# Kernel tuning notes

Hardware: AMD Instinct MI355X
Metric: run time of the kernel (lower is better)

Reference implementation:

```python
import jax, jax.numpy as jnp
import numpy as np

N_NODES = 50000
EMBED = 64
N_EDGES = 1250000
N_USERS = 25000
BATCH, K = 1024, 100


def setup_inputs() -> dict:
    key = jax.random.key(0)
    ks = jax.random.split(key, 8)
    stdv = 1.0 / np.sqrt(EMBED)
    emb = jax.random.uniform(ks[0], (N_NODES, EMBED), jnp.float32, -stdv, stdv)
    # nn.Linear default init: U(-1/sqrt(fan_in), 1/sqrt(fan_in))
    lim = 1.0 / np.sqrt(EMBED)
    W0 = jax.random.uniform(ks[1], (EMBED, EMBED), jnp.float32, -lim, lim)
    b0 = jax.random.uniform(ks[2], (EMBED,), jnp.float32, -lim, lim)
    W1 = jax.random.uniform(ks[3], (EMBED, EMBED), jnp.float32, -lim, lim)
    b1 = jax.random.uniform(ks[4], (EMBED,), jnp.float32, -lim, lim)
    src = jax.random.randint(ks[5], (N_EDGES,), 0, N_NODES, jnp.int32)
    dst = jax.random.randint(ks[6], (N_EDGES,), 0, N_NODES, jnp.int32)
    user_index = jax.random.randint(ks[7], (BATCH, K), 0, N_USERS, jnp.int32)
    item_index = jax.random.randint(jax.random.fold_in(key, 99), (BATCH, K), 0, N_NODES, jnp.int32)
    return {"embeddings": emb, "W0": W0, "b0": b0, "W1": W1, "b1": b1,
            "src": src, "dst": dst, "user_index": user_index, "item_index": item_index}


def _mean_aggregate(h, src, dst):
    # copy_src gather + mailbox mean: mean of src features over incoming edges per dst
    msg_sum = jax.ops.segment_sum(h[src], dst, num_segments=N_NODES)  # [N, D]
    deg = jax.ops.segment_sum(jnp.ones((src.shape[0],), h.dtype), dst, num_segments=N_NODES)
    return msg_sum / jnp.maximum(deg, 1.0)[:, None]


def reference(embeddings, W0, b0, W1, b1, src, dst, user_index, item_index):
    h = embeddings
    for W, b in ((W0, b0), (W1, b1)):
        agg = _mean_aggregate(h, src, dst)          # [N, D] mean mailbox
        h = jnp.tanh(agg @ W.T + b)                  # NodeUpdate: Linear + Tanh
    user = h[user_index]                             # [B, K, D]
    item = h[item_index]                             # [B, K, D]
    score = jnp.sum(user * item, axis=2)             # [B, K]
    return score
```

## Files before the change

### kernel.cpp

```cpp
#include <hip/hip_runtime.h>

#define N_NODES 50000
#define N_EDGES 1250000
#define EMBED 64
#define N_PAIRS (1024 * 100)
#define BSHIFT 7
#define BSIZE 128
#define NBUCK 391
#define CB 153
#define LDS_CAP 4096
#define GEMV_BLKS ((N_NODES + 63) / 64)

__device__ inline float bf2f(unsigned short u) {
    return __uint_as_float(((unsigned)u) << 16);
}
__device__ inline unsigned short f2bf(float x) {
    unsigned u = __float_as_uint(x);
    u += 0x7FFF + ((u >> 16) & 1);
    return (unsigned short)(u >> 16);
}

__global__ __launch_bounds__(1024) void hist_kernel(const int* __restrict__ dst,
                                                    int* __restrict__ counts,
                                                    int* __restrict__ btot) {
    __shared__ int hl[NBUCK];
    int t = threadIdx.x, b = blockIdx.x;
    for (int i = t; i < NBUCK; i += 1024) hl[i] = 0;
    __syncthreads();
    #pragma unroll
    for (int rep = 0; rep < 2; ++rep) {
        int i4 = b * 2048 + rep * 1024 + t;
        if (i4 < N_EDGES / 4) {
            int4 d = ((const int4*)dst)[i4];
            atomicAdd(&hl[d.x >> BSHIFT], 1);
            atomicAdd(&hl[d.y >> BSHIFT], 1);
            atomicAdd(&hl[d.z >> BSHIFT], 1);
            atomicAdd(&hl[d.w >> BSHIFT], 1);
        }
    }
    __syncthreads();
    for (int i = t; i < NBUCK; i += 1024) {
        int v = hl[i];
        counts[i * CB + b] = v;
        if (v) atomicAdd(&btot[i], v);
    }
}

__global__ __launch_bounds__(512) void bscan_kernel(const int* __restrict__ btot,
                                                    int* __restrict__ base) {
    __shared__ int ws[8];
    int t = threadIdx.x, lane = t & 63, wid = t >> 6;
    int v = (t < NBUCK) ? btot[t] : 0;
    int incl = v;
    #pragma unroll
    for (int off = 1; off < 64; off <<= 1) {
        int o = __shfl_up(incl, off);
        if (lane >= off) incl += o;
    }
    if (lane == 63) ws[wid] = incl;
    __syncthreads();
    if (t < 8) {
        int x = ws[t];
        #pragma unroll
        for (int off = 1; off < 8; off <<= 1) {
            int o = __shfl_up(x, off);
            if (t >= off) x += o;
        }
        ws[t] = x;
    }
    __syncthreads();
    int ex = ((wid > 0) ? ws[wid - 1] : 0) + incl - v;
    if (t < NBUCK) base[t] = ex;
    if (t == 0) base[NBUCK] = N_EDGES;
}

__global__ __launch_bounds__(64) void offs_kernel(const int* __restrict__ counts,
                                                  const int* __restrict__ base,
                                                  int* __restrict__ offs) {
    int k = blockIdx.x, lane = threadIdx.x;
    const int* rowp = counts + (size_t)k * CB;
    int* orow = offs + (size_t)k * CB;
    int carry = base[k];
    #pragma unroll
    for (int tile = 0; tile < 3; ++tile) {
        int b = tile * 64 + lane;
        int v = (b < CB) ? rowp[b] : 0;
        int incl = v;
        #pragma unroll
        for (int off = 1; off < 64; off <<= 1) {
            int o = __shfl_up(incl, off);
            if (lane >= off) incl += o;
        }
        if (b < CB) orow[b] = carry + incl - v;
        carry += __shfl(incl, 63);
    }
}

__global__ __launch_bounds__(1024) void scatter_kernel(const int* __restrict__ src,
                                                       const int* __restrict__ dst,
                                                       const int* __restrict__ offs,
                                                       unsigned int* __restrict__ pairs) {
    __shared__ int cur[NBUCK];
    int t = threadIdx.x, b = blockIdx.x;
    for (int i = t; i < NBUCK; i += 1024) cur[i] = offs[i * CB + b];
    __syncthreads();
    #pragma unroll
    for (int rep = 0; rep < 2; ++rep) {
        int i4 = b * 2048 + rep * 1024 + t;
        if (i4 < N_EDGES / 4) {
            int4 s4 = ((const int4*)src)[i4];
            int4 d4 = ((const int4*)dst)[i4];
            int p;
            p = atomicAdd(&cur[d4.x >> BSHIFT], 1);
            pairs[p] = ((unsigned)(d4.x & (BSIZE - 1)) << 16) | (unsigned)s4.x;
            p = atomicAdd(&cur[d4.y >> BSHIFT], 1);
            pairs[p] = ((unsigned)(d4.y & (BSIZE - 1)) << 16) | (unsigned)s4.y;
            p = atomicAdd(&cur[d4.z >> BSHIFT], 1);
            pairs[p] = ((unsigned)(d4.z & (BSIZE - 1)) << 16) | (unsigned)s4.z;
            p = atomicAdd(&cur[d4.w >> BSHIFT], 1);
            pairs[p] = ((unsigned)(d4.w & (BSIZE - 1)) << 16) | (unsigned)s4.w;
        }
    }
}

#define SMEM_BYTES 33808
__global__ __launch_bounds__(256) void sortgemv_kernel(const unsigned int* __restrict__ pairs,
                                                       const int* __restrict__ base,
                                                       int* __restrict__ row,
                                                       int* __restrict__ col,
                                                       const float* __restrict__ emb,
                                                       const float* __restrict__ W,
                                                       unsigned short* __restrict__ g) {
    __shared__ __align__(16) char smem[SMEM_BYTES];
    int t = threadIdx.x;
    if (blockIdx.x < NBUCK) {
        unsigned* ebuf = (unsigned*)smem;
        int* staged    = (int*)(smem + 16384);
        int* hist      = (int*)(smem + 32768);
        int* cur       = (int*)(smem + 33280);
        int* wtot      = (int*)(smem + 33792);
        int k = blockIdx.x;
        int lane = t & 63, wid = t >> 6;
        int nstart = k * BSIZE;
        int nodes = min(BSIZE, N_NODES - nstart);
        int estart = base[k], eend = base[k + 1];
        int cnt = eend - estart;
        if (t < BSIZE) hist[t] = 0;
        __syncthreads();
        if (cnt <= LDS_CAP) {
            for (int i = t; i < cnt; i += 256) {
                unsigned w = pairs[estart + i];
                ebuf[i] = w;
                atomicAdd(&hist[w >> 16], 1);
            }
            __syncthreads();
            if (t < BSIZE) {
                int v = hist[t];
                int incl = v;
                #pragma unroll
                for (int off = 1; off < 64; off <<= 1) {
                    int o = __shfl_up(incl, off);
                    if (lane >= off) incl += o;
                }
                if (t == 63) *wtot = incl;
                __syncthreads();
                int ex = incl - v + ((wid == 1) ? *wtot : 0);
                cur[t] = ex;
                if (t < nodes) row[nstart + t] = estart + ex;
            } else {
                __syncthreads();
            }
            if (k == NBUCK - 1 && t == 0) row[N_NODES] = N_EDGES;
            __syncthreads();
            for (int i = t; i < cnt; i += 256) {
                unsigned w = ebuf[i];
                int pos = atomicAdd(&cur[w >> 16], 1);
                staged[pos] = (int)(w & 0xFFFFu);
            }
            __syncthreads();
            for (int i = t; i < cnt; i += 256) col[estart + i] = staged[i];
        } else {
            for (int i = t; i < cnt; i += 256)
                atomicAdd(&hist[pairs[estart + i] >> 16], 1);
            __syncthreads();
            if (t < BSIZE) {
                int v = hist[t];
                int incl = v;
                #pragma unroll
                for (int off = 1; off < 64; off <<= 1) {
                    int o = __shfl_up(incl, off);
                    if (lane >= off) incl += o;
                }
                if (t == 63) *wtot = incl;
                __syncthreads();
                int ex = incl - v + ((wid == 1) ? *wtot : 0);
                cur[t] = ex;
                if (t < nodes) row[nstart + t] = estart + ex;
            } else {
                __syncthreads();
            }
            if (k == NBUCK - 1 && t == 0) row[N_NODES] = N_EDGES;
            __syncthreads();
            for (int i = t; i < cnt; i += 256) {
                unsigned w = pairs[estart + i];
                int pos = atomicAdd(&cur[w >> 16], 1);
                col[estart + pos] = (int)(w & 0xFFFFu);
            }
        }
    } else {
        float (*hL)[64] = (float (*)[64])smem;
        float (*Wl)[65] = (float (*)[65])(smem + 16384);
        int nstart = (blockIdx.x - NBUCK) * 64;
        int lane = t & 63, wid = t >> 6;
        for (int i = t; i < 4096; i += 256) Wl[i & 63][i >> 6] = W[i];
        int nrem = min(64, N_NODES - nstart);
        for (int i = t; i < nrem * 16; i += 256)
            ((float4*)hL)[i] = ((const float4*)(emb + (size_t)nstart * EMBED))[i];
        __syncthreads();
        for (int n = wid; n < nrem; n += 4) {
            float x = 0.f;
            #pragma unroll
            for (int d = 0; d < 64; ++d)
                x += hL[n][d] * Wl[d][lane];
            g[(size_t)(nstart + n) * EMBED + lane] = f2bf(x);
        }
    }
}

__global__ __launch_bounds__(256) void gemv_bf16_kernel(const unsigned short* __restrict__ h,
                                                        const float* __restrict__ W,
                                                        unsigned short* __restrict__ g) {
    __shared__ float hL[64][64];
    __shared__ float Wl[64][65];
    int t = threadIdx.x;
    int nstart = blockIdx.x * 64;
    int lane = t & 63, wid = t >> 6;
    for (int i = t; i < 4096; i += 256) Wl[i & 63][i >> 6] = W[i];
    int nrem = min(64, N_NODES - nstart);
    for (int i = t; i < nrem * 16; i += 256) {
        ushort4 v = ((const ushort4*)(h + (size_t)nstart * EMBED))[i];
        int r = i >> 4, c = (i & 15) * 4;
        hL[r][c + 0] = bf2f(v.x);
        hL[r][c + 1] = bf2f(v.y);
        hL[r][c + 2] = bf2f(v.z);
        hL[r][c + 3] = bf2f(v.w);
    }
    __syncthreads();
    for (int n = wid; n < nrem; n += 4) {
        float x = 0.f;
        #pragma unroll
        for (int d = 0; d < 64; ++d)
            x += hL[n][d] * Wl[d][lane];
        g[(size_t)(nstart + n) * EMBED + lane] = f2bf(x);
    }
}

__global__ __launch_bounds__(256) void agg_kernel(const unsigned short* __restrict__ g,
                                                  const float* __restrict__ bias,
                                                  const int* __restrict__ row,
                                                  const int* __restrict__ col,
                                                  unsigned short* __restrict__ hout) {
    int t = threadIdx.x;
    int wid = t >> 6, lane = t & 63;
    int node = blockIdx.x * 4 + wid;
    int gg = lane >> 4, d16 = lane & 15;
    int start = row[node], end = row[node + 1];
    float4 bb = ((const float4*)bias)[d16];
    float4 acc = {0.f, 0.f, 0.f, 0.f};
    for (int e = start; e < end; e += 32) {
        #pragma unroll
        for (int k = 0; k < 8; ++k) {
            int ee = e + 4 * k + gg;
            if (ee < end) {
                int s = col[ee];
                ushort4 v = ((const ushort4*)(g + (size_t)s * EMBED))[d16];
                acc.x += bf2f(v.x);
                acc.y += bf2f(v.y);
                acc.z += bf2f(v.z);
                acc.w += bf2f(v.w);
            }
        }
    }
    #pragma unroll
    for (int off = 16; off < 64; off <<= 1) {
        acc.x += __shfl_xor(acc.x, off);
        acc.y += __shfl_xor(acc.y, off);
        acc.z += __shfl_xor(acc.z, off);
        acc.w += __shfl_xor(acc.w, off);
    }
    int dg = end - start;
    float inv = (dg > 0) ? 1.0f / (float)dg : 0.f;
    if (gg == 0) {
        ushort4 o;
        o.x = f2bf(tanhf(acc.x * inv + bb.x));
        o.y = f2bf(tanhf(acc.y * inv + bb.y));
        o.z = f2bf(tanhf(acc.z * inv + bb.z));
        o.w = f2bf(tanhf(acc.w * inv + bb.w));
        ((ushort4*)(hout + (size_t)node * EMBED))[d16] = o;
    }
}

__global__ __launch_bounds__(256) void score_kernel(const unsigned short* __restrict__ h,
                                                    const int* __restrict__ ui,
                                                    const int* __restrict__ ii,
                                                    float* __restrict__ out) {
    int t = threadIdx.x;
    int idx = blockIdx.x * 16 + (t >> 4);
    int d16 = t & 15;
    int u = ui[idx];
    int v = ii[idx];
    ushort4 a4 = ((const ushort4*)(h + (size_t)u * EMBED))[d16];
    ushort4 b4 = ((const ushort4*)(h + (size_t)v * EMBED))[d16];
    float p = bf2f(a4.x) * bf2f(b4.x) + bf2f(a4.y) * bf2f(b4.y) +
              bf2f(a4.z) * bf2f(b4.z) + bf2f(a4.w) * bf2f(b4.w);
    #pragma unroll
    for (int off = 8; off > 0; off >>= 1)
        p += __shfl_xor(p, off);
    if (d16 == 0) out[idx] = p;
}

extern "C" void kernel_launch(void* const* d_in, const int* in_sizes, int n_in,
                              void* d_out, int out_size, void* d_ws, size_t ws_size,
                              hipStream_t stream) {
    const float* emb = (const float*)d_in[0];
    const float* W0  = (const float*)d_in[1];
    const float* b0  = (const float*)d_in[2];
    const float* W1  = (const float*)d_in[3];
    const float* b1  = (const float*)d_in[4];
    const int* src   = (const int*)d_in[5];
    const int* dst   = (const int*)d_in[6];
    const int* ui    = (const int*)d_in[7];
    const int* ii    = (const int*)d_in[8];
    float* out = (float*)d_out;

    char* p = (char*)d_ws;
    auto alloc = [&](size_t bytes) {
        char* r = p;
        p += (bytes + 255) & ~(size_t)255;
        return r;
    };
    int* counts          = (int*)alloc(sizeof(int) * NBUCK * CB);
    int* offs            = (int*)alloc(sizeof(int) * NBUCK * CB);
    int* btot            = (int*)alloc(sizeof(int) * NBUCK);
    int* base            = (int*)alloc(sizeof(int) * (NBUCK + 1));
    int* row             = (int*)alloc(sizeof(int) * (N_NODES + 1));
    unsigned* pairs      = (unsigned*)alloc(sizeof(unsigned) * N_EDGES);
    int* col             = (int*)alloc(sizeof(int) * N_EDGES);
    unsigned short* gbuf = (unsigned short*)alloc(sizeof(unsigned short) * N_NODES * EMBED);
    unsigned short* hbuf = (unsigned short*)alloc(sizeof(unsigned short) * N_NODES * EMBED);

    hipMemsetAsync(btot, 0, sizeof(int) * NBUCK, stream);
    hist_kernel<<<CB, 1024, 0, stream>>>(dst, counts, btot);
    bscan_kernel<<<1, 512, 0, stream>>>(btot, base);
    offs_kernel<<<NBUCK, 64, 0, stream>>>(counts, base, offs);
    scatter_kernel<<<CB, 1024, 0, stream>>>(src, dst, offs, pairs);
    sortgemv_kernel<<<NBUCK + GEMV_BLKS, 256, 0, stream>>>(pairs, base, row, col,
                                                           emb, W0, gbuf);
    agg_kernel<<<N_NODES / 4, 256, 0, stream>>>(gbuf, b0, row, col, hbuf);
    gemv_bf16_kernel<<<GEMV_BLKS, 256, 0, stream>>>(hbuf, W1, gbuf);
    agg_kernel<<<N_NODES / 4, 256, 0, stream>>>(gbuf, b1, row, col, hbuf);
    score_kernel<<<N_PAIRS / 16, 256, 0, stream>>>(hbuf, ui, ii, out);
}
```

Baseline: 245.9 us.

## Switch intermediates to fp32 and pad CSR rows to multiples of four

Drops the bf16 storage of the transformed features and hidden states and keeps everything in fp32. The CSR layout now gives each bucket a fixed region and pads every node's edge list to a multiple of four, filling the padding with a dummy node whose feature row is zero. This removes the per-edge bounds checks in the aggregation loop, which now processes eight edges per step unguarded. The cost is twice the gather bytes from fp32 features, a larger col buffer, and a padding fill pass in the sort kernel.

```diff
diff --git a/kernel.cpp b/kernel.cpp
--- a/kernel.cpp
+++ b/kernel.cpp
@@ -9,16 +9,9 @@
 #define NBUCK 391
 #define CB 153
 #define LDS_CAP 4096
+#define FAST_MAX 3584
+#define CAP 4096
 #define GEMV_BLKS ((N_NODES + 63) / 64)
-
-__device__ inline float bf2f(unsigned short u) {
-    return __uint_as_float(((unsigned)u) << 16);
-}
-__device__ inline unsigned short f2bf(float x) {
-    unsigned u = __float_as_uint(x);
-    u += 0x7FFF + ((u >> 16) & 1);
-    return (unsigned short)(u >> 16);
-}
 
 __global__ __launch_bounds__(1024) void hist_kernel(const int* __restrict__ dst,
                                                     int* __restrict__ counts,
@@ -123,14 +116,15 @@
     }
 }
 
-#define SMEM_BYTES 33808
+#define SMEM_BYTES 34832
 __global__ __launch_bounds__(256) void sortgemv_kernel(const unsigned int* __restrict__ pairs,
                                                        const int* __restrict__ base,
-                                                       int* __restrict__ row,
+                                                       int* __restrict__ rowp,
+                                                       int* __restrict__ degv,
                                                        int* __restrict__ col,
                                                        const float* __restrict__ emb,
                                                        const float* __restrict__ W,
-                                                       unsigned short* __restrict__ g) {
+                                                       float* __restrict__ g) {
     __shared__ __align__(16) char smem[SMEM_BYTES];
     int t = threadIdx.x;
     if (blockIdx.x < NBUCK) {
@@ -139,15 +133,17 @@
         int* hist      = (int*)(smem + 32768);
         int* cur       = (int*)(smem + 33280);
         int* wtot      = (int*)(smem + 33792);
+        int* ptotS     = (int*)(smem + 33796);
         int k = blockIdx.x;
         int lane = t & 63, wid = t >> 6;
         int nstart = k * BSIZE;
         int nodes = min(BSIZE, N_NODES - nstart);
         int estart = base[k], eend = base[k + 1];
         int cnt = eend - estart;
+        int cbase = k << 12;
         if (t < BSIZE) hist[t] = 0;
         __syncthreads();
-        if (cnt <= LDS_CAP) {
+        if (cnt <= FAST_MAX) {
             for (int i = t; i < cnt; i += 256) {
                 unsigned w = pairs[estart + i];
                 ebuf[i] = w;
@@ -155,8 +151,9 @@
             }
             __syncthreads();
             if (t < BSIZE) {
-                int v = hist[t];
-                int incl = v;
+                int dgv = hist[t];
+                int pd = (dgv + 3) & ~3;
+                int incl = pd;
                 #pragma unroll
                 for (int off = 1; off < 64; off <<= 1) {
                     int o = __shfl_up(incl, off);
@@ -164,13 +161,19 @@
                 }
                 if (t == 63) *wtot = incl;
                 __syncthreads();
-                int ex = incl - v + ((wid == 1) ? *wtot : 0);
+                int ex = incl - pd + ((wid == 1) ? *wtot : 0);
                 cur[t] = ex;
-                if (t < nodes) row[nstart + t] = estart + ex;
+                if (t == BSIZE - 1) *ptotS = ex + pd;
+                if (t < nodes) {
+                    rowp[nstart + t] = cbase + ex;
+                    degv[nstart + t] = dgv;
+                }
             } else {
                 __syncthreads();
             }
-            if (k == NBUCK - 1 && t == 0) row[N_NODES] = N_EDGES;
+            __syncthreads();
+            int ptot = *ptotS;
+            for (int i = t; i < ptot; i += 256) staged[i] = N_NODES;
             __syncthreads();
             for (int i = t; i < cnt; i += 256) {
                 unsigned w = ebuf[i];
@@ -178,14 +181,15 @@
                 staged[pos] = (int)(w & 0xFFFFu);
             }
             __syncthreads();
-            for (int i = t; i < cnt; i += 256) col[estart + i] = staged[i];
+            for (int i = t; i < ptot; i += 256) col[cbase + i] = staged[i];
         } else {
             for (int i = t; i < cnt; i += 256)
                 atomicAdd(&hist[pairs[estart + i] >> 16], 1);
             __syncthreads();
             if (t < BSIZE) {
-                int v = hist[t];
-                int incl = v;
+                int dgv = hist[t];
+                int pd = (dgv + 3) & ~3;
+                int incl = pd;
                 #pragma unroll
                 for (int off = 1; off < 64; off <<= 1) {
                     int o = __shfl_up(incl, off);
@@ -193,43 +197,51 @@
                 }
                 if (t == 63) *wtot = incl;
                 __syncthreads();
-                int ex = incl - v + ((wid == 1) ? *wtot : 0);
+                int ex = incl - pd + ((wid == 1) ? *wtot : 0);
                 cur[t] = ex;
-                if (t < nodes) row[nstart + t] = estart + ex;
+                if (t == BSIZE - 1) *ptotS = ex + pd;
+                if (t < nodes) {
+                    rowp[nstart + t] = cbase + ex;
+                    degv[nstart + t] = dgv;
+                }
             } else {
                 __syncthreads();
             }
-            if (k == NBUCK - 1 && t == 0) row[N_NODES] = N_EDGES;
+            __syncthreads();
+            int ptot = *ptotS;
+            for (int i = t; i < ptot; i += 256) col[cbase + i] = N_NODES;
             __syncthreads();
             for (int i = t; i < cnt; i += 256) {
                 unsigned w = pairs[estart + i];
                 int pos = atomicAdd(&cur[w >> 16], 1);
-                col[estart + pos] = (int)(w & 0xFFFFu);
+                col[cbase + pos] = (int)(w & 0xFFFFu);
             }
         }
     } else {
         float (*hL)[64] = (float (*)[64])smem;
         float (*Wl)[65] = (float (*)[65])(smem + 16384);
-        int nstart = (blockIdx.x - NBUCK) * 64;
+        int gb = blockIdx.x - NBUCK;
+        int nstart = gb * 64;
         int lane = t & 63, wid = t >> 6;
         for (int i = t; i < 4096; i += 256) Wl[i & 63][i >> 6] = W[i];
         int nrem = min(64, N_NODES - nstart);
         for (int i = t; i < nrem * 16; i += 256)
             ((float4*)hL)[i] = ((const float4*)(emb + (size_t)nstart * EMBED))[i];
+        if (gb == GEMV_BLKS - 1 && t < 64) g[(size_t)N_NODES * EMBED + t] = 0.f;
         __syncthreads();
         for (int n = wid; n < nrem; n += 4) {
             float x = 0.f;
             #pragma unroll
             for (int d = 0; d < 64; ++d)
                 x += hL[n][d] * Wl[d][lane];
-            g[(size_t)(nstart + n) * EMBED + lane] = f2bf(x);
-        }
-    }
-}
-
-__global__ __launch_bounds__(256) void gemv_bf16_kernel(const unsigned short* __restrict__ h,
-                                                        const float* __restrict__ W,
-                                                        unsigned short* __restrict__ g) {
+            g[(size_t)(nstart + n) * EMBED + lane] = x;
+        }
+    }
+}
+
+__global__ __launch_bounds__(256) void gemv_kernel(const float* __restrict__ h,
+                                                   const float* __restrict__ W,
+                                                   float* __restrict__ g) {
     __shared__ float hL[64][64];
     __shared__ float Wl[64][65];
     int t = threadIdx.x;
@@ -237,49 +249,49 @@
     int lane = t & 63, wid = t >> 6;
     for (int i = t; i < 4096; i += 256) Wl[i & 63][i >> 6] = W[i];
     int nrem = min(64, N_NODES - nstart);
-    for (int i = t; i < nrem * 16; i += 256) {
-        ushort4 v = ((const ushort4*)(h + (size_t)nstart * EMBED))[i];
-        int r = i >> 4, c = (i & 15) * 4;
-        hL[r][c + 0] = bf2f(v.x);
-        hL[r][c + 1] = bf2f(v.y);
-        hL[r][c + 2] = bf2f(v.z);
-        hL[r][c + 3] = bf2f(v.w);
-    }
+    for (int i = t; i < nrem * 16; i += 256)
+        ((float4*)hL)[i] = ((const float4*)(h + (size_t)nstart * EMBED))[i];
     __syncthreads();
     for (int n = wid; n < nrem; n += 4) {
         float x = 0.f;
         #pragma unroll
         for (int d = 0; d < 64; ++d)
             x += hL[n][d] * Wl[d][lane];
-        g[(size_t)(nstart + n) * EMBED + lane] = f2bf(x);
-    }
-}
-
-__global__ __launch_bounds__(256) void agg_kernel(const unsigned short* __restrict__ g,
+        g[(size_t)(nstart + n) * EMBED + lane] = x;
+    }
+}
+
+__global__ __launch_bounds__(256) void agg_kernel(const float* __restrict__ g,
                                                   const float* __restrict__ bias,
-                                                  const int* __restrict__ row,
+                                                  const int* __restrict__ rowp,
+                                                  const int* __restrict__ degv,
                                                   const int* __restrict__ col,
-                                                  unsigned short* __restrict__ hout) {
+                                                  float* __restrict__ hout) {
     int t = threadIdx.x;
     int wid = t >> 6, lane = t & 63;
     int node = blockIdx.x * 4 + wid;
     int gg = lane >> 4, d16 = lane & 15;
-    int start = row[node], end = row[node + 1];
+    int start = rowp[node];
+    int dg = degv[node];
+    int pcnt = (dg + 3) & ~3;
+    int endp = start + pcnt;
     float4 bb = ((const float4*)bias)[d16];
     float4 acc = {0.f, 0.f, 0.f, 0.f};
-    for (int e = start; e < end; e += 32) {
-        #pragma unroll
-        for (int k = 0; k < 8; ++k) {
-            int ee = e + 4 * k + gg;
-            if (ee < end) {
-                int s = col[ee];
-                ushort4 v = ((const ushort4*)(g + (size_t)s * EMBED))[d16];
-                acc.x += bf2f(v.x);
-                acc.y += bf2f(v.y);
-                acc.z += bf2f(v.z);
-                acc.w += bf2f(v.w);
-            }
-        }
+    int e = start;
+    for (; e + 8 <= endp; e += 8) {
+        int s0 = col[e + gg];
+        int s1 = col[e + 4 + gg];
+        float4 v0 = ((const float4*)(g + (size_t)s0 * EMBED))[d16];
+        float4 v1 = ((const float4*)(g + (size_t)s1 * EMBED))[d16];
+        acc.x += v0.x + v1.x;
+        acc.y += v0.y + v1.y;
+        acc.z += v0.z + v1.z;
+        acc.w += v0.w + v1.w;
+    }
+    if (e < endp) {
+        int s0 = col[e + gg];
+        float4 v0 = ((const float4*)(g + (size_t)s0 * EMBED))[d16];
+        acc.x += v0.x; acc.y += v0.y; acc.z += v0.z; acc.w += v0.w;
     }
     #pragma unroll
     for (int off = 16; off < 64; off <<= 1) {
@@ -288,19 +300,18 @@
         acc.z += __shfl_xor(acc.z, off);
         acc.w += __shfl_xor(acc.w, off);
     }
-    int dg = end - start;
     float inv = (dg > 0) ? 1.0f / (float)dg : 0.f;
     if (gg == 0) {
-        ushort4 o;
-        o.x = f2bf(tanhf(acc.x * inv + bb.x));
-        o.y = f2bf(tanhf(acc.y * inv + bb.y));
-        o.z = f2bf(tanhf(acc.z * inv + bb.z));
-        o.w = f2bf(tanhf(acc.w * inv + bb.w));
-        ((ushort4*)(hout + (size_t)node * EMBED))[d16] = o;
-    }
-}
-
-__global__ __launch_bounds__(256) void score_kernel(const unsigned short* __restrict__ h,
+        float4 o;
+        o.x = tanhf(acc.x * inv + bb.x);
+        o.y = tanhf(acc.y * inv + bb.y);
+        o.z = tanhf(acc.z * inv + bb.z);
+        o.w = tanhf(acc.w * inv + bb.w);
+        ((float4*)(hout + (size_t)node * EMBED))[d16] = o;
+    }
+}
+
+__global__ __launch_bounds__(256) void score_kernel(const float* __restrict__ h,
                                                     const int* __restrict__ ui,
                                                     const int* __restrict__ ii,
                                                     float* __restrict__ out) {
@@ -309,10 +320,9 @@
     int d16 = t & 15;
     int u = ui[idx];
     int v = ii[idx];
-    ushort4 a4 = ((const ushort4*)(h + (size_t)u * EMBED))[d16];
-    ushort4 b4 = ((const ushort4*)(h + (size_t)v * EMBED))[d16];
-    float p = bf2f(a4.x) * bf2f(b4.x) + bf2f(a4.y) * bf2f(b4.y) +
-              bf2f(a4.z) * bf2f(b4.z) + bf2f(a4.w) * bf2f(b4.w);
+    float4 a = ((const float4*)(h + (size_t)u * EMBED))[d16];
+    float4 b = ((const float4*)(h + (size_t)v * EMBED))[d16];
+    float p = a.x * b.x + a.y * b.y + a.z * b.z + a.w * b.w;
     #pragma unroll
     for (int off = 8; off > 0; off >>= 1)
         p += __shfl_xor(p, off);
@@ -339,25 +349,26 @@
         p += (bytes + 255) & ~(size_t)255;
         return r;
     };
-    int* counts          = (int*)alloc(sizeof(int) * NBUCK * CB);
-    int* offs            = (int*)alloc(sizeof(int) * NBUCK * CB);
-    int* btot            = (int*)alloc(sizeof(int) * NBUCK);
-    int* base            = (int*)alloc(sizeof(int) * (NBUCK + 1));
-    int* row             = (int*)alloc(sizeof(int) * (N_NODES + 1));
-    unsigned* pairs      = (unsigned*)alloc(sizeof(unsigned) * N_EDGES);
-    int* col             = (int*)alloc(sizeof(int) * N_EDGES);
-    unsigned short* gbuf = (unsigned short*)alloc(sizeof(unsigned short) * N_NODES * EMBED);
-    unsigned short* hbuf = (unsigned short*)alloc(sizeof(unsigned short) * N_NODES * EMBED);
+    int* counts     = (int*)alloc(sizeof(int) * NBUCK * CB);
+    int* offs       = (int*)alloc(sizeof(int) * NBUCK * CB);
+    int* btot       = (int*)alloc(sizeof(int) * NBUCK);
+    int* base       = (int*)alloc(sizeof(int) * (NBUCK + 1));
+    int* rowp       = (int*)alloc(sizeof(int) * N_NODES);
+    int* degv       = (int*)alloc(sizeof(int) * N_NODES);
+    unsigned* pairs = (unsigned*)alloc(sizeof(unsigned) * N_EDGES);
+    int* col        = (int*)alloc(sizeof(int) * NBUCK * CAP);
+    float* gbuf     = (float*)alloc(sizeof(float) * (N_NODES + 1) * EMBED);
+    float* hbuf     = (float*)alloc(sizeof(float) * N_NODES * EMBED);
 
     hipMemsetAsync(btot, 0, sizeof(int) * NBUCK, stream);
     hist_kernel<<<CB, 1024, 0, stream>>>(dst, counts, btot);
     bscan_kernel<<<1, 512, 0, stream>>>(btot, base);
     offs_kernel<<<NBUCK, 64, 0, stream>>>(counts, base, offs);
     scatter_kernel<<<CB, 1024, 0, stream>>>(src, dst, offs, pairs);
-    sortgemv_kernel<<<NBUCK + GEMV_BLKS, 256, 0, stream>>>(pairs, base, row, col,
+    sortgemv_kernel<<<NBUCK + GEMV_BLKS, 256, 0, stream>>>(pairs, base, rowp, degv, col,
                                                            emb, W0, gbuf);
-    agg_kernel<<<N_NODES / 4, 256, 0, stream>>>(gbuf, b0, row, col, hbuf);
-    gemv_bf16_kernel<<<GEMV_BLKS, 256, 0, stream>>>(hbuf, W1, gbuf);
-    agg_kernel<<<N_NODES / 4, 256, 0, stream>>>(gbuf, b1, row, col, hbuf);
+    agg_kernel<<<N_NODES / 4, 256, 0, stream>>>(gbuf, b0, rowp, degv, col, hbuf);
+    gemv_kernel<<<GEMV_BLKS, 256, 0, stream>>>(hbuf, W1, gbuf);
+    agg_kernel<<<N_NODES / 4, 256, 0, stream>>>(gbuf, b1, rowp, degv, col, hbuf);
     score_kernel<<<N_PAIRS / 16, 256, 0, stream>>>(hbuf, ui, ii, out);
 }
```

After: 240.3 us. 1.02x faster.
